# Kernel tuning notes

Hardware: AMD Instinct MI355X
Metric: run time of the kernel (lower is better)

The kernel has to match this reference:

```python
import jax, jax.numpy as jnp
import numpy as np

B, V, T = 8, 16, 64
DIN, H, RH, K, TMP = 6, 256, 64, 2, 256
E = V * (V - 1)
NREL, NPOS = 7, 3  # 2D relative / positional feature counts

_edges = np.ones((V, V)) - np.eye(V)
SEND = jnp.asarray(np.where(_edges)[0])
RECV = jnp.asarray(np.where(_edges)[1])


def _w(k, shape, fan):
    return jax.random.normal(k, shape, jnp.float32) / np.sqrt(fan)


def setup_inputs() -> dict:
    key = jax.random.key(0)
    ks = jax.random.split(key, 20)
    d = {}
    d['rel_feat'] = jax.random.normal(ks[0], (B, V, T, DIN), jnp.float32)
    d['edge_attr_raw'] = jax.random.normal(ks[1], (B, E, T, NREL + DIN), jnp.float32)
    d['edge_pos'] = jax.random.normal(ks[2], (B, E, T, NPOS), jnp.float32)
    d['ef_w1'] = _w(ks[3], (H, NREL + DIN + NPOS), NREL + DIN + NPOS); d['ef_b1'] = jnp.full((H,), 0.1)
    d['ef_w2'] = _w(ks[4], (H, H), H); d['ef_b2'] = jnp.full((H,), 0.1)
    d['res_w'] = _w(ks[5], (H, DIN), DIN); d['res_b'] = jnp.full((H,), 0.1)
    d['m3_w1'] = _w(ks[6], (H, H), H); d['m3_b1'] = jnp.full((H,), 0.1)
    d['m3_w2'] = _w(ks[7], (H, H), H); d['m3_b2'] = jnp.full((H,), 0.1)
    d['m4_w1'] = _w(ks[8], (H, 3 * H), 3 * H); d['m4_b1'] = jnp.full((H,), 0.1)
    d['m4_w2'] = _w(ks[9], (H, H), H); d['m4_b2'] = jnp.full((H,), 0.1)
    d['f_wih'] = _w(ks[10], (4 * RH, H), H); d['f_whh'] = _w(ks[11], (4 * RH, RH), RH)
    d['f_bih'] = jnp.zeros((4 * RH,)); d['f_bhh'] = jnp.zeros((4 * RH,))
    d['r_wih'] = _w(ks[12], (4 * RH, H), H); d['r_whh'] = _w(ks[13], (4 * RH, RH), RH)
    d['r_bih'] = jnp.zeros((4 * RH,)); d['r_bhh'] = jnp.zeros((4 * RH,))
    d['p_w'] = _w(ks[14], (K, RH), RH); d['p_b'] = jnp.full((K,), 0.1)
    d['e_w1'] = _w(ks[15], (TMP, 2 * RH), 2 * RH); d['e_b1'] = jnp.full((TMP,), 0.1)
    d['e_w2'] = _w(ks[16], (K, TMP), TMP); d['e_b2'] = jnp.full((K,), 0.1)
    return d


def _lstm(x, wih, whh, bih, bhh):
    # x: [N, T, H] -> hidden sequence [N, T, RH]; torch gate order i, f, g, o
    n = x.shape[0]
    rh = whh.shape[1]
    xw = jnp.einsum('nth,gh->ntg', x, wih) + bih  # input GEMM hoisted out of scan

    def step(carry, xt):
        h, c = carry
        z = xt + h @ whh.T + bhh
        i, f, g, o = jnp.split(z, 4, axis=-1)
        c = jax.nn.sigmoid(f) * c + jax.nn.sigmoid(i) * jnp.tanh(g)
        h = jax.nn.sigmoid(o) * jnp.tanh(c)
        return (h, c), h

    h0 = jnp.zeros((n, rh), x.dtype)
    _, hs = jax.lax.scan(step, (h0, h0), jnp.swapaxes(xw, 0, 1))
    return jnp.swapaxes(hs, 0, 1)


def reference(rel_feat, edge_attr_raw, edge_pos, ef_w1, ef_b1, ef_w2, ef_b2, res_w, res_b, m3_w1, m3_b1, m3_w2, m3_b2, m4_w1, m4_b1, m4_w2, m4_b2, f_wih, f_whh, f_bih, f_bhh, r_wih, r_whh, r_bih, r_bhh, p_w, p_b, e_w1, e_b1, e_w2, e_b2):
    elu = jax.nn.elu
    # edge filter MLP: [B,E,T,NREL+DIN+NPOS] -> [B,E,T,H]
    ein = jnp.concatenate([edge_attr_raw, edge_pos], -1)
    edge_attr = elu(elu(ein @ ef_w1.T + ef_b1) @ ef_w2.T + ef_b2)
    # edge2node: scatter-sum over recv indices, normalized by (V-1)
    agg = jax.ops.segment_sum(jnp.moveaxis(edge_attr, 1, 0), RECV, num_segments=V)
    x = jnp.moveaxis(agg, 0, 1) / (V - 1) + (rel_feat @ res_w.T + res_b)
    # mlp3 on node embeddings
    x = elu(elu(x @ m3_w1.T + m3_b1) @ m3_w2.T + m3_b2)
    # node2edge gather + skip-concat with previous edge features -> mlp4
    x = jnp.concatenate([x[:, SEND], x[:, RECV], edge_attr], -1)  # [B,E,T,3H]
    x = elu(elu(x @ m4_w1.T + m4_b1) @ m4_w2.T + m4_b2)  # [B,E,T,H]
    # bidirectional LSTM over time, per edge
    seq = x.reshape(B * E, T, H)
    fwd = _lstm(seq, f_wih, f_whh, f_bih, f_bhh)
    rev = jnp.flip(_lstm(jnp.flip(seq, 1), r_wih, r_whh, r_bih, r_bhh), 1)
    prior = (fwd @ p_w.T + p_b).reshape(B, E, T, K).transpose(0, 2, 1, 3)  # [B,T,E,K]
    comb = jnp.concatenate([fwd, rev], -1)
    enc = (elu(comb @ e_w1.T + e_b1) @ e_w2.T + e_b2).reshape(B, E, T, K).transpose(0, 2, 1, 3)
    return prior, enc
```

## Files before the change

kernel.cpp:

```cpp
#include <hip/hip_runtime.h>
#include <cstdint>
#include <cstddef>
#include <type_traits>

#define B_ 8
#define V_ 16
#define T_ 64
#define E_ 240
#define H_ 256
#define RH_ 64
#define K_ 2
#define DIN_ 6
#define BET_ (B_*E_*T_)
#define BVT_ (B_*V_*T_)
#define BE_ (B_*E_)

typedef unsigned short ushort_t;
typedef unsigned int u32;
typedef __attribute__((ext_vector_type(8))) short bf16x8;
typedef __attribute__((ext_vector_type(4))) float f32x4;

__device__ __forceinline__ float eluf(float x) { return x > 0.f ? x : __expf(x) - 1.f; }
__device__ __forceinline__ float fsig(float x) { return 1.f / (1.f + __expf(-x)); }
__device__ __forceinline__ float ftanh_(float x) {
    float y = fminf(fmaxf(x, -8.f), 8.f);
    float e = __expf(2.f * y);
    return (e - 1.f) / (e + 1.f);
}
__device__ __forceinline__ float b2f(ushort_t u) {
    union { float f; uint32_t i; } v; v.i = ((uint32_t)u) << 16; return v.f;
}
__device__ __forceinline__ ushort_t f2b(float f) {
    union { float f; uint32_t i; } v; v.f = f;
    uint32_t r = (v.i + 0x7FFFu + ((v.i >> 16) & 1u)) >> 16;
    return (ushort_t)r;
}

__device__ __forceinline__ void gll16(const void* g, void* l) {
    __builtin_amdgcn_global_load_lds(
        (const __attribute__((address_space(1))) u32*)g,
        (__attribute__((address_space(3))) u32*)l, 16, 0, 0);
}

template<int KD, int ACT>
__global__ __launch_bounds__(512, 2) void gemm8_k(
    const ushort_t* __restrict__ A, const ushort_t* __restrict__ Wt,
    const float* __restrict__ b1, const float* __restrict__ b2,
    ushort_t* __restrict__ C)
{
    __shared__ ushort_t lds[4][32][512];
    const int tid = threadIdx.x;
    const int lane = tid & 63;
    const int w = tid >> 6;
    const int wm = w >> 2, wn = w & 3;
    const int m0 = blockIdx.x * 256;
    const int r16 = lane & 15, kq = lane >> 4;
    constexpr int NH = KD / 32;

    const ushort_t* Ag0 = A + (size_t)(m0 + w * 16 + r16) * KD + kq * 8;
    const ushort_t* Ag1 = A + (size_t)(m0 + (w + 8) * 16 + r16) * KD + kq * 8;
    const ushort_t* Bg0 = Wt + (size_t)(w * 16 + r16) * KD + kq * 8;
    const ushort_t* Bg1 = Wt + (size_t)((w + 8) * 16 + r16) * KD + kq * 8;

    f32x4 acc[8][4];
    #pragma unroll
    for (int i = 0; i < 8; ++i)
        #pragma unroll
        for (int j = 0; j < 4; ++j)
            acc[i][j] = (f32x4){0.f, 0.f, 0.f, 0.f};

#define ST8(h) do { int sl_ = (h) & 3; int kk_ = (h) * 32;                  \
    gll16(Ag0 + kk_, &lds[sl_][w][0]);                                      \
    gll16(Ag1 + kk_, &lds[sl_][w + 8][0]);                                  \
    gll16(Bg0 + kk_, &lds[sl_][16 + w][0]);                                 \
    gll16(Bg1 + kk_, &lds[sl_][16 + w + 8][0]);                             \
} while (0)

    ST8(0); ST8(1); ST8(2);
    asm volatile("s_waitcnt vmcnt(8)" ::: "memory");
    __builtin_amdgcn_s_barrier();

    for (int h = 0; h < NH; ++h) {
        if (h + 3 < NH) ST8(h + 3);
        const int sl = h & 3;
        bf16x8 bfr[4];
        #pragma unroll
        for (int nf = 0; nf < 4; ++nf)
            bfr[nf] = *(const bf16x8*)&lds[sl][16 + wn * 4 + nf][lane * 8];
        #pragma unroll
        for (int mh = 0; mh < 2; ++mh) {
            bf16x8 af[4];
            #pragma unroll
            for (int mf = 0; mf < 4; ++mf)
                af[mf] = *(const bf16x8*)&lds[sl][wm * 8 + mh * 4 + mf][lane * 8];
            __builtin_amdgcn_s_setprio(1);
            #pragma unroll
            for (int mf = 0; mf < 4; ++mf)
                #pragma unroll
                for (int nf = 0; nf < 4; ++nf)
                    acc[mh * 4 + mf][nf] = __builtin_amdgcn_mfma_f32_16x16x32_bf16(
                        bfr[nf], af[mf], acc[mh * 4 + mf][nf], 0, 0, 0);
            __builtin_amdgcn_s_setprio(0);
        }
        asm volatile("s_waitcnt lgkmcnt(0)" ::: "memory");
        if (h < NH - 3)       { asm volatile("s_waitcnt vmcnt(8)" ::: "memory"); }
        else if (h == NH - 3) { asm volatile("s_waitcnt vmcnt(4)" ::: "memory"); }
        else if (h == NH - 2) { asm volatile("s_waitcnt vmcnt(0)" ::: "memory"); }
        if (h < NH - 1) __builtin_amdgcn_s_barrier();
    }
#undef ST8

    #pragma unroll
    for (int mi = 0; mi < 8; ++mi) {
        int mrow = m0 + wm * 128 + mi * 16 + r16;
        #pragma unroll
        for (int nf = 0; nf < 4; ++nf) {
            int nb = wn * 64 + nf * 16 + kq * 4;
            float4 bb = *(const float4*)&b1[nb];
            if (b2) {
                float4 b2v = *(const float4*)&b2[nb];
                bb.x += b2v.x; bb.y += b2v.y; bb.z += b2v.z; bb.w += b2v.w;
            }
            float v0 = acc[mi][nf][0] + bb.x;
            float v1 = acc[mi][nf][1] + bb.y;
            float v2 = acc[mi][nf][2] + bb.z;
            float v3 = acc[mi][nf][3] + bb.w;
            if (ACT) { v0 = eluf(v0); v1 = eluf(v1); v2 = eluf(v2); v3 = eluf(v3); }
            ushort4 o; o.x = f2b(v0); o.y = f2b(v1); o.z = f2b(v2); o.w = f2b(v3);
            *(ushort4*)&C[(size_t)mrow * 256 + nb] = o;
        }
    }
}

__global__ __launch_bounds__(512, 2) void gemm8_mlp4_k(
    const ushort_t* __restrict__ X2b, const ushort_t* __restrict__ EA,
    const ushort_t* __restrict__ Wt, const float* __restrict__ b1,
    ushort_t* __restrict__ C)
{
    __shared__ ushort_t lds[4][32][512];
    const int tid = threadIdx.x;
    const int lane = tid & 63;
    const int w = tid >> 6;
    const int wm = w >> 2, wn = w & 3;
    const int m0 = blockIdx.x * 256;
    const int r16 = lane & 15, kq = lane >> 4;
    constexpr int NH = 24;

    const ushort_t* AS[2]; const ushort_t* AR[2]; const ushort_t* AE[2];
    #pragma unroll
    for (int ff = 0; ff < 2; ++ff) {
        int f = w + ff * 8;
        int m = m0 + f * 16 + r16;
        int be = m >> 6, t = m & 63;
        int b = be / E_, e = be % E_;
        int s = e / (V_ - 1);
        int r0 = e % (V_ - 1);
        int rr = r0 + (r0 >= s ? 1 : 0);
        AS[ff] = X2b + ((size_t)((b * V_ + s) * T_ + t)) * H_ + kq * 8;
        AR[ff] = X2b + ((size_t)((b * V_ + rr) * T_ + t)) * H_ + kq * 8;
        AE[ff] = EA + (size_t)m * H_ + kq * 8;
    }
    const ushort_t* Bg0 = Wt + (size_t)(w * 16 + r16) * 768 + kq * 8;
    const ushort_t* Bg1 = Wt + (size_t)((w + 8) * 16 + r16) * 768 + kq * 8;

    f32x4 acc[8][4];
    #pragma unroll
    for (int i = 0; i < 8; ++i)
        #pragma unroll
        for (int j = 0; j < 4; ++j)
            acc[i][j] = (f32x4){0.f, 0.f, 0.f, 0.f};

#define STM(h) do { int sl_ = (h) & 3; int kk_ = (h) * 32;                  \
    int seg_ = kk_ >> 8, off_ = kk_ & 255;                                  \
    const ushort_t* a0_ = (seg_ == 0 ? AS[0] : seg_ == 1 ? AR[0] : AE[0]) + off_; \
    const ushort_t* a1_ = (seg_ == 0 ? AS[1] : seg_ == 1 ? AR[1] : AE[1]) + off_; \
    gll16(a0_, &lds[sl_][w][0]);                                            \
    gll16(a1_, &lds[sl_][w + 8][0]);                                        \
    gll16(Bg0 + kk_, &lds[sl_][16 + w][0]);                                 \
    gll16(Bg1 + kk_, &lds[sl_][16 + w + 8][0]);                             \
} while (0)

    STM(0); STM(1); STM(2);
    asm volatile("s_waitcnt vmcnt(8)" ::: "memory");
    __builtin_amdgcn_s_barrier();

    for (int h = 0; h < NH; ++h) {
        if (h + 3 < NH) STM(h + 3);
        const int sl = h & 3;
        bf16x8 bfr[4];
        #pragma unroll
        for (int nf = 0; nf < 4; ++nf)
            bfr[nf] = *(const bf16x8*)&lds[sl][16 + wn * 4 + nf][lane * 8];
        #pragma unroll
        for (int mh = 0; mh < 2; ++mh) {
            bf16x8 af[4];
            #pragma unroll
            for (int mf = 0; mf < 4; ++mf)
                af[mf] = *(const bf16x8*)&lds[sl][wm * 8 + mh * 4 + mf][lane * 8];
            __builtin_amdgcn_s_setprio(1);
            #pragma unroll
            for (int mf = 0; mf < 4; ++mf)
                #pragma unroll
                for (int nf = 0; nf < 4; ++nf)
                    acc[mh * 4 + mf][nf] = __builtin_amdgcn_mfma_f32_16x16x32_bf16(
                        bfr[nf], af[mf], acc[mh * 4 + mf][nf], 0, 0, 0);
            __builtin_amdgcn_s_setprio(0);
        }
        asm volatile("s_waitcnt lgkmcnt(0)" ::: "memory");
        if (h < NH - 3)       { asm volatile("s_waitcnt vmcnt(8)" ::: "memory"); }
        else if (h == NH - 3) { asm volatile("s_waitcnt vmcnt(4)" ::: "memory"); }
        else if (h == NH - 2) { asm volatile("s_waitcnt vmcnt(0)" ::: "memory"); }
        if (h < NH - 1) __builtin_amdgcn_s_barrier();
    }
#undef STM

    #pragma unroll
    for (int mi = 0; mi < 8; ++mi) {
        int mrow = m0 + wm * 128 + mi * 16 + r16;
        #pragma unroll
        for (int nf = 0; nf < 4; ++nf) {
            int nb = wn * 64 + nf * 16 + kq * 4;
            float4 bb = *(const float4*)&b1[nb];
            float v0 = eluf(acc[mi][nf][0] + bb.x);
            float v1 = eluf(acc[mi][nf][1] + bb.y);
            float v2 = eluf(acc[mi][nf][2] + bb.z);
            float v3 = eluf(acc[mi][nf][3] + bb.w);
            ushort4 o; o.x = f2b(v0); o.y = f2b(v1); o.z = f2b(v2); o.w = f2b(v3);
            *(ushort4*)&C[(size_t)mrow * 256 + nb] = o;
        }
    }
}

__global__ __launch_bounds__(256) void wconv_k(
    const float* __restrict__ ef_w2, const float* __restrict__ m4_w1,
    const float* __restrict__ m4_w2, const float* __restrict__ f_wih,
    const float* __restrict__ r_wih, const float* __restrict__ e_w1,
    ushort_t* __restrict__ Wb)
{
    int i = blockIdx.x * 256 + threadIdx.x;
    const float* src; int off;
    if (i < 65536)       { src = ef_w2; off = i; }
    else if (i < 262144) { src = m4_w1; off = i - 65536; }
    else if (i < 327680) { src = m4_w2; off = i - 262144; }
    else if (i < 393216) { src = f_wih; off = i - 327680; }
    else if (i < 458752) { src = r_wih; off = i - 393216; }
    else                 { src = e_w1;  off = i - 458752; }
    Wb[i] = f2b(src[off]);
}

template<typename TA, typename TO>
__global__ __launch_bounds__(256) void gemm_t(
    const TA* __restrict__ A, const float* __restrict__ W,
    const float* __restrict__ b1, const float* __restrict__ b2,
    TO* __restrict__ C, int M, int Kd, int N, int act)
{
    __shared__ float As[16][64];
    __shared__ float Ws[16][64];
    const int m0 = blockIdx.x * 64, n0 = blockIdx.y * 64;
    const int tid = threadIdx.x;
    const int tm = tid >> 4, tn = tid & 15;
    const int lm = tid >> 2, lq = tid & 3;
    float acc[4][4] = {};
    const TA* Arow = A + (size_t)(m0 + lm) * Kd + lq * 4;
    const float* Wrow = W + (size_t)(n0 + lm) * Kd + lq * 4;
    for (int k0 = 0; k0 < Kd; k0 += 16) {
        float4 av, wv;
        if constexpr (std::is_same<TA, ushort_t>::value) {
            ushort4 u = *(const ushort4*)(Arow + k0);
            av.x = b2f(u.x); av.y = b2f(u.y); av.z = b2f(u.z); av.w = b2f(u.w);
        } else {
            av = *(const float4*)(Arow + k0);
        }
        wv = *(const float4*)(Wrow + k0);
        __syncthreads();
        As[lq*4+0][lm] = av.x; As[lq*4+1][lm] = av.y; As[lq*4+2][lm] = av.z; As[lq*4+3][lm] = av.w;
        Ws[lq*4+0][lm] = wv.x; Ws[lq*4+1][lm] = wv.y; Ws[lq*4+2][lm] = wv.z; Ws[lq*4+3][lm] = wv.w;
        __syncthreads();
        #pragma unroll
        for (int k = 0; k < 16; ++k) {
            float4 a = *(const float4*)&As[k][tm * 4];
            float4 w = *(const float4*)&Ws[k][tn * 4];
            float a_[4] = {a.x, a.y, a.z, a.w};
            float w_[4] = {w.x, w.y, w.z, w.w};
            #pragma unroll
            for (int i = 0; i < 4; ++i)
                #pragma unroll
                for (int j = 0; j < 4; ++j)
                    acc[i][j] += a_[i] * w_[j];
        }
    }
    float bb[4];
    #pragma unroll
    for (int j = 0; j < 4; ++j) {
        int n = n0 + tn * 4 + j;
        bb[j] = b1[n] + (b2 ? b2[n] : 0.f);
    }
    #pragma unroll
    for (int i = 0; i < 4; ++i) {
        float v0 = acc[i][0] + bb[0], v1 = acc[i][1] + bb[1];
        float v2 = acc[i][2] + bb[2], v3 = acc[i][3] + bb[3];
        if (act) { v0 = eluf(v0); v1 = eluf(v1); v2 = eluf(v2); v3 = eluf(v3); }
        TO* dst = C + (size_t)(m0 + tm * 4 + i) * N + (n0 + tn * 4);
        if constexpr (std::is_same<TO, ushort_t>::value) {
            ushort4 o; o.x = f2b(v0); o.y = f2b(v1); o.z = f2b(v2); o.w = f2b(v3);
            *(ushort4*)dst = o;
        } else {
            float4 o; o.x = v0; o.y = v1; o.z = v2; o.w = v3;
            *(float4*)dst = o;
        }
    }
}

__global__ __launch_bounds__(256) void gemm_ein_k(
    const float* __restrict__ ear, const float* __restrict__ epos,
    const float* __restrict__ W, const float* __restrict__ b1,
    ushort_t* __restrict__ C)
{
    __shared__ float As[16][64];
    __shared__ float Ws[16][64];
    const int m0 = blockIdx.x * 64, n0 = blockIdx.y * 64;
    const int tid = threadIdx.x;
    const int tm = tid >> 4, tn = tid & 15;
    const int lm = tid >> 2, lq = tid & 3;
    const int m = m0 + lm;
    float a_[4];
    #pragma unroll
    for (int q = 0; q < 4; ++q) {
        int c = lq * 4 + q;
        a_[q] = (c < 13) ? ear[(size_t)m * 13 + c] : epos[(size_t)m * 3 + (c - 13)];
    }
    float4 wv = *(const float4*)(W + (size_t)(n0 + lm) * 16 + lq * 4);
    As[lq*4+0][lm] = a_[0]; As[lq*4+1][lm] = a_[1]; As[lq*4+2][lm] = a_[2]; As[lq*4+3][lm] = a_[3];
    Ws[lq*4+0][lm] = wv.x; Ws[lq*4+1][lm] = wv.y; Ws[lq*4+2][lm] = wv.z; Ws[lq*4+3][lm] = wv.w;
    __syncthreads();
    float acc[4][4] = {};
    #pragma unroll
    for (int k = 0; k < 16; ++k) {
        float4 a = *(const float4*)&As[k][tm * 4];
        float4 w = *(const float4*)&Ws[k][tn * 4];
        float aa[4] = {a.x, a.y, a.z, a.w};
        float ww[4] = {w.x, w.y, w.z, w.w};
        #pragma unroll
        for (int i = 0; i < 4; ++i)
            #pragma unroll
            for (int j = 0; j < 4; ++j)
                acc[i][j] += aa[i] * ww[j];
    }
    #pragma unroll
    for (int i = 0; i < 4; ++i) {
        ushort4 o;
        o.x = f2b(eluf(acc[i][0] + b1[n0 + tn*4 + 0]));
        o.y = f2b(eluf(acc[i][1] + b1[n0 + tn*4 + 1]));
        o.z = f2b(eluf(acc[i][2] + b1[n0 + tn*4 + 2]));
        o.w = f2b(eluf(acc[i][3] + b1[n0 + tn*4 + 3]));
        *(ushort4*)(C + (size_t)(m0 + tm * 4 + i) * H_ + (n0 + tn * 4)) = o;
    }
}

__global__ __launch_bounds__(256) void e2n_k(
    const ushort_t* __restrict__ EA, const float* __restrict__ rel,
    const float* __restrict__ res_w, const float* __restrict__ res_b,
    float* __restrict__ X)
{
    const int idx = blockIdx.x;
    const int t = idx & (T_ - 1);
    const int bv = idx >> 6;
    const int v = bv & (V_ - 1);
    const int b = bv >> 4;
    const int h = threadIdx.x;
    float sum = 0.f;
    #pragma unroll
    for (int i = 0; i < V_; ++i) {
        if (i == v) continue;
        int jj = (v < i) ? v : v - 1;
        int e = i * (V_ - 1) + jj;
        sum += b2f(EA[(((size_t)(b * E_ + e)) * T_ + t) * H_ + h]);
    }
    const float* rp = rel + ((size_t)bv * T_ + t) * DIN_;
    float res = res_b[h];
    #pragma unroll
    for (int d = 0; d < DIN_; ++d) res += rp[d] * res_w[h * DIN_ + d];
    X[((size_t)bv * T_ + t) * H_ + h] = sum * (1.f / 15.f) + res;
}

__global__ __launch_bounds__(256) void lstm_mfma4_k(
    const ushort_t* __restrict__ G, const float* __restrict__ whh,
    ushort_t* __restrict__ COMB, int dir)
{
    __shared__ ushort_t hlds[2][1024];
    const int tid = threadIdx.x;
    const int lane = tid & 63;
    const int w = tid >> 6;
    const int seq = lane & 15, kq = lane >> 4;
    const int be0 = blockIdx.x * 16;
    const int swz = (seq & 7) << 4;

    bf16x8 wf[4][2];
    #pragma unroll
    for (int a = 0; a < 4; ++a) {
        #pragma unroll
        for (int ks = 0; ks < 2; ++ks) {
            const float* p = whh + (size_t)((a * 4 + w) * 16 + seq) * 64 + ks * 32 + kq * 8;
            float4 x0 = *(const float4*)p;
            float4 x1 = *(const float4*)(p + 4);
            bf16x8 v;
            v[0] = (short)f2b(x0.x); v[1] = (short)f2b(x0.y);
            v[2] = (short)f2b(x0.z); v[3] = (short)f2b(x0.w);
            v[4] = (short)f2b(x1.x); v[5] = (short)f2b(x1.y);
            v[6] = (short)f2b(x1.z); v[7] = (short)f2b(x1.w);
            wf[a][ks] = v;
        }
    }

    const ushort_t* grow = G + ((size_t)(be0 + seq) * T_) * 256 + kq * 4;
    ushort_t* crow = COMB + ((size_t)(be0 + seq) * T_) * 128 + (dir ? 64 : 0) + 16 * w + 4 * kq;

    float c[4] = {};
    ushort4 gx[4];
    const int t0 = dir ? (T_ - 1) : 0;
    #pragma unroll
    for (int a = 0; a < 4; ++a)
        gx[a] = *(const ushort4*)(grow + (size_t)t0 * 256 + (a * 4 + w) * 16);

    for (int s = 0; s < T_; ++s) {
        const int t = dir ? (T_ - 1 - s) : s;
        f32x4 acc[4];
        #pragma unroll
        for (int a = 0; a < 4; ++a) {
            ushort4 g = gx[a];
            acc[a] = (f32x4){b2f(g.x), b2f(g.y), b2f(g.z), b2f(g.w)};
        }
        if (s < T_ - 1) {
            const int tn = dir ? (T_ - 2 - s) : (s + 1);
            #pragma unroll
            for (int a = 0; a < 4; ++a)
                gx[a] = *(const ushort4*)(grow + (size_t)tn * 256 + (a * 4 + w) * 16);
        }
        if (s) {
            bf16x8 af[2];
            #pragma unroll
            for (int ks = 0; ks < 2; ++ks) {
                int boff = (seq * 128 + ks * 64 + kq * 16) ^ swz;
                af[ks] = *(const bf16x8*)((const char*)hlds[(s - 1) & 1] + boff);
            }
            #pragma unroll
            for (int a = 0; a < 4; ++a) {
                acc[a] = __builtin_amdgcn_mfma_f32_16x16x32_bf16(wf[a][0], af[0], acc[a], 0, 0, 0);
                acc[a] = __builtin_amdgcn_mfma_f32_16x16x32_bf16(wf[a][1], af[1], acc[a], 0, 0, 0);
            }
        }
        float hh[4];
        #pragma unroll
        for (int r = 0; r < 4; ++r) {
            float zi = acc[0][r], zf = acc[1][r], zg = acc[2][r], zo = acc[3][r];
            float cc = fsig(zf) * c[r] + fsig(zi) * ftanh_(zg);
            c[r] = cc;
            hh[r] = fsig(zo) * ftanh_(cc);
        }
        ushort4 hv;
        hv.x = f2b(hh[0]); hv.y = f2b(hh[1]); hv.z = f2b(hh[2]); hv.w = f2b(hh[3]);
        int wb = (seq * 128 + 32 * w + 8 * kq) ^ swz;
        *(ushort4*)((char*)hlds[s & 1] + wb) = hv;
        *(ushort4*)(crow + (size_t)t * 128) = hv;
        asm volatile("s_waitcnt lgkmcnt(0)" ::: "memory");
        __builtin_amdgcn_sched_barrier(0);
        __builtin_amdgcn_s_barrier();
    }
}

__global__ __launch_bounds__(256) void prior_k(
    const ushort_t* __restrict__ COMB, const float* __restrict__ p_w,
    const float* __restrict__ p_b, float* __restrict__ out)
{
    const int row = blockIdx.x * 4 + (threadIdx.x >> 6);
    const int lane = threadIdx.x & 63;
    float hf = b2f(COMB[(size_t)row * 128 + lane]);
    float v0 = hf * p_w[lane];
    float v1 = hf * p_w[64 + lane];
    #pragma unroll
    for (int off = 32; off > 0; off >>= 1) {
        v0 += __shfl_down(v0, off, 64);
        v1 += __shfl_down(v1, off, 64);
    }
    if (lane == 0) {
        int t = row & (T_ - 1);
        int be = row >> 6;
        int e = be % E_, b = be / E_;
        size_t o = (((size_t)b * T_ + t) * E_ + e) * K_;
        out[o] = v0 + p_b[0];
        out[o + 1] = v1 + p_b[1];
    }
}

__global__ __launch_bounds__(512) void fused_enc_k(
    const ushort_t* __restrict__ COMB, const ushort_t* __restrict__ w_e1,
    const float* __restrict__ e_b1, const float* __restrict__ e_w2,
    const float* __restrict__ e_b2, float* __restrict__ out)
{
    __shared__ ushort_t sA[2][8][512];
    __shared__ ushort_t sW[2][16][512];
    __shared__ float part[128][4][2];
    const int tid = threadIdx.x;
    const int lane = tid & 63;
    const int w = tid >> 6;
    const int wr = w >> 2, wc = w & 3;
    const int m0 = blockIdx.x * 128;
    const int r16 = lane & 15, kq = lane >> 4;

    const ushort_t* Asrc = COMB + (size_t)(m0 + w * 16 + r16) * 128 + kq * 8;
    const size_t woffA = (size_t)((2 * w) * 16 + r16) * 128 + kq * 8;
    const size_t woffB = (size_t)((2 * w + 1) * 16 + r16) * 128 + kq * 8;

    float4 w2v[2][4];
    #pragma unroll
    for (int j = 0; j < 2; ++j)
        #pragma unroll
        for (int nf = 0; nf < 4; ++nf)
            w2v[j][nf] = *(const float4*)&e_w2[j * 256 + wc * 64 + nf * 16 + kq * 4];

    f32x4 acc[4][4];
    #pragma unroll
    for (int i = 0; i < 4; ++i)
        #pragma unroll
        for (int j = 0; j < 4; ++j)
            acc[i][j] = (f32x4){0.f, 0.f, 0.f, 0.f};

#define FE_STAGE(bufi, kt_) do {                                             \
    gll16(Asrc + (kt_) * 32, &sA[bufi][w][0]);                               \
    gll16(w_e1 + woffA + (kt_) * 32, &sW[bufi][2 * w][0]);                   \
    gll16(w_e1 + woffB + (kt_) * 32, &sW[bufi][2 * w + 1][0]);               \
} while (0)

    FE_STAGE(0, 0);
    asm volatile("s_waitcnt vmcnt(0)" ::: "memory");
    __builtin_amdgcn_s_barrier();

    for (int s = 0; s < 4; ++s) {
        const int buf = s & 1;
        if (s < 3) FE_STAGE(buf ^ 1, s + 1);
        bf16x8 af[4], bfr[4];
        #pragma unroll
        for (int mf = 0; mf < 4; ++mf)
            af[mf] = *(const bf16x8*)&sA[buf][wr * 4 + mf][lane * 8];
        #pragma unroll
        for (int nf = 0; nf < 4; ++nf)
            bfr[nf] = *(const bf16x8*)&sW[buf][wc * 4 + nf][lane * 8];
        #pragma unroll
        for (int mf = 0; mf < 4; ++mf)
            #pragma unroll
            for (int nf = 0; nf < 4; ++nf)
                acc[mf][nf] = __builtin_amdgcn_mfma_f32_16x16x32_bf16(bfr[nf], af[mf], acc[mf][nf], 0, 0, 0);
        asm volatile("s_waitcnt vmcnt(0)" ::: "memory");
        __builtin_amdgcn_s_barrier();
    }

    #pragma unroll
    for (int mf = 0; mf < 4; ++mf) {
        float s0 = 0.f, s1 = 0.f;
        #pragma unroll
        for (int nf = 0; nf < 4; ++nf) {
            int col = wc * 64 + nf * 16 + kq * 4;
            float4 bb = *(const float4*)&e_b1[col];
            float v0 = eluf(acc[mf][nf][0] + bb.x);
            float v1 = eluf(acc[mf][nf][1] + bb.y);
            float v2 = eluf(acc[mf][nf][2] + bb.z);
            float v3 = eluf(acc[mf][nf][3] + bb.w);
            s0 += v0 * w2v[0][nf].x + v1 * w2v[0][nf].y + v2 * w2v[0][nf].z + v3 * w2v[0][nf].w;
            s1 += v0 * w2v[1][nf].x + v1 * w2v[1][nf].y + v2 * w2v[1][nf].z + v3 * w2v[1][nf].w;
        }
        s0 += __shfl_xor(s0, 16, 64); s0 += __shfl_xor(s0, 32, 64);
        s1 += __shfl_xor(s1, 16, 64); s1 += __shfl_xor(s1, 32, 64);
        if (kq == 0) {
            part[wr * 64 + mf * 16 + r16][wc][0] = s0;
            part[wr * 64 + mf * 16 + r16][wc][1] = s1;
        }
    }
    __syncthreads();
    if (tid < 256) {
        int row = tid >> 1, k = tid & 1;
        float v = part[row][0][k] + part[row][1][k] + part[row][2][k] + part[row][3][k] + e_b2[k];
        int gr = m0 + row;
        int be = gr >> 6, t = gr & 63;
        int e = be % E_, b = be / E_;
        out[(size_t)(B_ * T_ * E_ * K_) + (((size_t)b * T_ + t) * E_ + e) * K_ + k] = v;
    }
#undef FE_STAGE
}

extern "C" void kernel_launch(void* const* d_in, const int* in_sizes, int n_in,
                              void* d_out, int out_size, void* d_ws, size_t ws_size,
                              hipStream_t stream)
{
    const float* rel    = (const float*)d_in[0];
    const float* ear    = (const float*)d_in[1];
    const float* epos   = (const float*)d_in[2];
    const float* ef_w1  = (const float*)d_in[3];
    const float* ef_b1  = (const float*)d_in[4];
    const float* ef_w2  = (const float*)d_in[5];
    const float* ef_b2  = (const float*)d_in[6];
    const float* res_w  = (const float*)d_in[7];
    const float* res_b  = (const float*)d_in[8];
    const float* m3_w1  = (const float*)d_in[9];
    const float* m3_b1  = (const float*)d_in[10];
    const float* m3_w2  = (const float*)d_in[11];
    const float* m3_b2  = (const float*)d_in[12];
    const float* m4_w1  = (const float*)d_in[13];
    const float* m4_b1  = (const float*)d_in[14];
    const float* m4_w2  = (const float*)d_in[15];
    const float* m4_b2  = (const float*)d_in[16];
    const float* f_wih  = (const float*)d_in[17];
    const float* f_whh  = (const float*)d_in[18];
    const float* f_bih  = (const float*)d_in[19];
    const float* f_bhh  = (const float*)d_in[20];
    const float* r_wih  = (const float*)d_in[21];
    const float* r_whh  = (const float*)d_in[22];
    const float* r_bih  = (const float*)d_in[23];
    const float* r_bhh  = (const float*)d_in[24];
    const float* p_w    = (const float*)d_in[25];
    const float* p_b    = (const float*)d_in[26];
    const float* e_w1   = (const float*)d_in[27];
    const float* e_b1   = (const float*)d_in[28];
    const float* e_w2   = (const float*)d_in[29];
    const float* e_b2   = (const float*)d_in[30];
    float* out = (float*)d_out;

    char* ws = (char*)d_ws;
    const size_t BIGB  = (size_t)BET_ * H_ * sizeof(ushort_t);
    const size_t COMBB = (size_t)BET_ * 128 * sizeof(ushort_t);
    const size_t X2BB  = (size_t)BVT_ * H_ * sizeof(ushort_t);
    ushort_t* R1   = (ushort_t*)(ws);
    ushort_t* R2   = (ushort_t*)(ws + BIGB);
    ushort_t* COMB = (ushort_t*)(ws + 2 * BIGB);
    ushort_t* X2b  = (ushort_t*)(ws + 2 * BIGB + COMBB);
    ushort_t* Wb   = (ushort_t*)(ws + 2 * BIGB + COMBB + X2BB);
    float* X  = (float*)(ws);
    float* XH = (float*)(ws + (size_t)BVT_ * H_ * sizeof(float));
    const ushort_t* wb_ef2  = Wb + 0;
    const ushort_t* wb_m41  = Wb + 65536;
    const ushort_t* wb_m42  = Wb + 262144;
    const ushort_t* wb_fwih = Wb + 327680;
    const ushort_t* wb_rwih = Wb + 393216;
    const ushort_t* wb_ew1  = Wb + 458752;

    dim3 blk(256);
    dim3 blk8(512);
    dim3 g8(BET_ / 256);
    dim3 gE64(BET_ / 64, 4);
    dim3 gN(BVT_ / 64, 4);

    wconv_k<<<1920, blk, 0, stream>>>(ef_w2, m4_w1, m4_w2, f_wih, r_wih, e_w1, Wb);
    gemm_ein_k<<<gE64, blk, 0, stream>>>(ear, epos, ef_w1, ef_b1, R1);
    gemm8_k<256, 1><<<g8, blk8, 0, stream>>>(R1, wb_ef2, ef_b2, nullptr, R2);
    e2n_k<<<BVT_, blk, 0, stream>>>(R2, rel, res_w, res_b, X);
    gemm_t<float, float><<<gN, blk, 0, stream>>>(X, m3_w1, m3_b1, nullptr, XH, BVT_, H_, H_, 1);
    gemm_t<float, ushort_t><<<gN, blk, 0, stream>>>(XH, m3_w2, m3_b2, nullptr, X2b, BVT_, H_, H_, 1);
    gemm8_mlp4_k<<<g8, blk8, 0, stream>>>(X2b, R2, wb_m41, m4_b1, R1);
    gemm8_k<256, 1><<<g8, blk8, 0, stream>>>(R1, wb_m42, m4_b2, nullptr, R2);
    gemm8_k<256, 0><<<g8, blk8, 0, stream>>>(R2, wb_fwih, f_bih, f_bhh, R1);
    lstm_mfma4_k<<<BE_ / 16, blk, 0, stream>>>(R1, f_whh, COMB, 0);
    gemm8_k<256, 0><<<g8, blk8, 0, stream>>>(R2, wb_rwih, r_bih, r_bhh, R1);
    lstm_mfma4_k<<<BE_ / 16, blk, 0, stream>>>(R1, r_whh, COMB, 1);
    prior_k<<<BET_ / 4, blk, 0, stream>>>(COMB, p_w, p_b, out);
    fused_enc_k<<<BET_ / 128, blk8, 0, stream>>>(COMB, wb_ew1, e_b1, e_w2, e_b2, out);
}
```

Before: 493.9 us.

## Fuse edge-filter MLP, mlp4 second layer with both LSTM input GEMMs, merge LSTM launches

Replaces the separate edge-filter first-layer GEMM and second-layer GEMM with one kernel that computes layer one with MFMA and keeps it in LDS. It also fuses the mlp4 second layer with the forward and reverse LSTM input-projection GEMMs, keeping the intermediate in LDS rather than writing it to global memory. The two LSTM direction launches are merged into a single grid with blockIdx.y selecting the direction. The aim is to cut global round-trips of 61k-row activation tensors and kernel launches, and to let both directions run concurrently. In exchange, tiles shrink to 128 rows with occupancy 1, and the fused kernel writes in place into its input buffer T1.

```diff
diff --git a/kernel.cpp b/kernel.cpp
--- a/kernel.cpp
+++ b/kernel.cpp
@@ -42,94 +42,273 @@
         (__attribute__((address_space(3))) u32*)l, 16, 0, 0);
 }
 
-template<int KD, int ACT>
-__global__ __launch_bounds__(512, 2) void gemm8_k(
-    const ushort_t* __restrict__ A, const ushort_t* __restrict__ Wt,
-    const float* __restrict__ b1, const float* __restrict__ b2,
-    ushort_t* __restrict__ C)
-{
-    __shared__ ushort_t lds[4][32][512];
+__global__ __launch_bounds__(512, 1) void gemm8_ef_k(
+    const float* __restrict__ ear, const float* __restrict__ epos,
+    const float* __restrict__ ef_w1, const float* __restrict__ ef_b1,
+    const ushort_t* __restrict__ w_ef2, const float* __restrict__ ef_b2,
+    ushort_t* __restrict__ EA)
+{
+    __shared__ ushort_t H1[8][8][512];
+    __shared__ ushort_t slotB[4][16][512];
     const int tid = threadIdx.x;
     const int lane = tid & 63;
     const int w = tid >> 6;
     const int wm = w >> 2, wn = w & 3;
-    const int m0 = blockIdx.x * 256;
+    const int m0 = blockIdx.x * 128;
     const int r16 = lane & 15, kq = lane >> 4;
-    constexpr int NH = KD / 32;
-
-    const ushort_t* Ag0 = A + (size_t)(m0 + w * 16 + r16) * KD + kq * 8;
-    const ushort_t* Ag1 = A + (size_t)(m0 + (w + 8) * 16 + r16) * KD + kq * 8;
-    const ushort_t* Bg0 = Wt + (size_t)(w * 16 + r16) * KD + kq * 8;
-    const ushort_t* Bg1 = Wt + (size_t)((w + 8) * 16 + r16) * KD + kq * 8;
-
-    f32x4 acc[8][4];
-    #pragma unroll
-    for (int i = 0; i < 8; ++i)
+
+    f32x4 acc[4][4];
+    #pragma unroll
+    for (int i = 0; i < 4; ++i)
         #pragma unroll
         for (int j = 0; j < 4; ++j)
             acc[i][j] = (f32x4){0.f, 0.f, 0.f, 0.f};
-
-#define ST8(h) do { int sl_ = (h) & 3; int kk_ = (h) * 32;                  \
-    gll16(Ag0 + kk_, &lds[sl_][w][0]);                                      \
-    gll16(Ag1 + kk_, &lds[sl_][w + 8][0]);                                  \
-    gll16(Bg0 + kk_, &lds[sl_][16 + w][0]);                                 \
-    gll16(Bg1 + kk_, &lds[sl_][16 + w + 8][0]);                             \
+    {
+        bf16x8 af[4], bfr[4];
+        #pragma unroll
+        for (int mf = 0; mf < 4; ++mf) {
+            int m = m0 + wm * 64 + mf * 16 + r16;
+            #pragma unroll
+            for (int e = 0; e < 8; ++e) {
+                float v = 0.f;
+                if (kq < 2) {
+                    int c = kq * 8 + e;
+                    v = (c < 13) ? ear[(size_t)m * 13 + c] : epos[(size_t)m * 3 + (c - 13)];
+                }
+                af[mf][e] = (short)f2b(v);
+            }
+        }
+        #pragma unroll
+        for (int nf = 0; nf < 4; ++nf) {
+            int n = wn * 64 + nf * 16 + r16;
+            #pragma unroll
+            for (int e = 0; e < 8; ++e) {
+                float v = 0.f;
+                if (kq < 2) v = ef_w1[(size_t)n * 16 + kq * 8 + e];
+                bfr[nf][e] = (short)f2b(v);
+            }
+        }
+        #pragma unroll
+        for (int mf = 0; mf < 4; ++mf)
+            #pragma unroll
+            for (int nf = 0; nf < 4; ++nf)
+                acc[mf][nf] = __builtin_amdgcn_mfma_f32_16x16x32_bf16(bfr[nf], af[mf], acc[mf][nf], 0, 0, 0);
+    }
+
+    const size_t bo0 = (size_t)(2 * w * 16 + r16) * 256 + kq * 8;
+    const size_t bo1 = (size_t)((2 * w + 1) * 16 + r16) * 256 + kq * 8;
+#define EF_ST(h) do { int sl_ = (h) & 3;                                    \
+    gll16(w_ef2 + bo0 + (h) * 32, &slotB[sl_][2 * w][0]);                   \
+    gll16(w_ef2 + bo1 + (h) * 32, &slotB[sl_][2 * w + 1][0]);               \
 } while (0)
 
-    ST8(0); ST8(1); ST8(2);
-    asm volatile("s_waitcnt vmcnt(8)" ::: "memory");
+    EF_ST(0); EF_ST(1); EF_ST(2);
+
+    #pragma unroll
+    for (int mf = 0; mf < 4; ++mf) {
+        #pragma unroll
+        for (int nf = 0; nf < 4; ++nf) {
+            int col = wn * 64 + nf * 16 + kq * 4;
+            float4 bb = *(const float4*)&ef_b1[col];
+            ushort4 o;
+            o.x = f2b(eluf(acc[mf][nf][0] + bb.x));
+            o.y = f2b(eluf(acc[mf][nf][1] + bb.y));
+            o.z = f2b(eluf(acc[mf][nf][2] + bb.z));
+            o.w = f2b(eluf(acc[mf][nf][3] + bb.w));
+            int ktw = wn * 2 + (nf >> 1);
+            int lanew = r16 + 16 * (((nf & 1) << 1) | (kq >> 1));
+            *(ushort4*)&H1[wm * 4 + mf][ktw][lanew * 8 + (kq & 1) * 4] = o;
+            acc[mf][nf] = (f32x4){0.f, 0.f, 0.f, 0.f};
+        }
+    }
+    asm volatile("s_waitcnt lgkmcnt(0)" ::: "memory");
+    asm volatile("s_waitcnt vmcnt(4)" ::: "memory");
     __builtin_amdgcn_s_barrier();
 
-    for (int h = 0; h < NH; ++h) {
-        if (h + 3 < NH) ST8(h + 3);
+    #pragma unroll
+    for (int h = 0; h < 8; ++h) {
+        if (h + 3 < 8) EF_ST(h + 3);
         const int sl = h & 3;
-        bf16x8 bfr[4];
+        bf16x8 af[4], bfr[4];
         #pragma unroll
         for (int nf = 0; nf < 4; ++nf)
-            bfr[nf] = *(const bf16x8*)&lds[sl][16 + wn * 4 + nf][lane * 8];
-        #pragma unroll
-        for (int mh = 0; mh < 2; ++mh) {
-            bf16x8 af[4];
+            bfr[nf] = *(const bf16x8*)&slotB[sl][wn * 4 + nf][lane * 8];
+        #pragma unroll
+        for (int mf = 0; mf < 4; ++mf)
+            af[mf] = *(const bf16x8*)&H1[wm * 4 + mf][h][lane * 8];
+        __builtin_amdgcn_s_setprio(1);
+        #pragma unroll
+        for (int mf = 0; mf < 4; ++mf)
+            #pragma unroll
+            for (int nf = 0; nf < 4; ++nf)
+                acc[mf][nf] = __builtin_amdgcn_mfma_f32_16x16x32_bf16(bfr[nf], af[mf], acc[mf][nf], 0, 0, 0);
+        __builtin_amdgcn_s_setprio(0);
+        asm volatile("s_waitcnt lgkmcnt(0)" ::: "memory");
+        if (h <= 4)      { asm volatile("s_waitcnt vmcnt(4)" ::: "memory"); }
+        else if (h == 5) { asm volatile("s_waitcnt vmcnt(2)" ::: "memory"); }
+        else if (h == 6) { asm volatile("s_waitcnt vmcnt(0)" ::: "memory"); }
+        if (h < 7) __builtin_amdgcn_s_barrier();
+    }
+#undef EF_ST
+
+    #pragma unroll
+    for (int mf = 0; mf < 4; ++mf) {
+        int row = m0 + wm * 64 + mf * 16 + r16;
+        #pragma unroll
+        for (int nf = 0; nf < 4; ++nf) {
+            int col = wn * 64 + nf * 16 + kq * 4;
+            float4 bb = *(const float4*)&ef_b2[col];
+            ushort4 o;
+            o.x = f2b(eluf(acc[mf][nf][0] + bb.x));
+            o.y = f2b(eluf(acc[mf][nf][1] + bb.y));
+            o.z = f2b(eluf(acc[mf][nf][2] + bb.z));
+            o.w = f2b(eluf(acc[mf][nf][3] + bb.w));
+            *(ushort4*)&EA[(size_t)row * 256 + col] = o;
+        }
+    }
+}
+
+__global__ __launch_bounds__(512, 1) void fused_gates8_k(
+    ushort_t* __restrict__ T1, ushort_t* __restrict__ GR,
+    const ushort_t* __restrict__ w_m42, const ushort_t* __restrict__ w_fih,
+    const ushort_t* __restrict__ w_rih, const float* __restrict__ m4_b2,
+    const float* __restrict__ f_bih, const float* __restrict__ f_bhh,
+    const float* __restrict__ r_bih, const float* __restrict__ r_bhh)
+{
+    __shared__ ushort_t M2[8][8][512];
+    __shared__ ushort_t slotA[3][8][512];
+    __shared__ ushort_t slotB[3][16][512];
+    const int tid = threadIdx.x;
+    const int lane = tid & 63;
+    const int w = tid >> 6;
+    const int wm = w >> 2, wn = w & 3;
+    const int m0 = blockIdx.x * 128;
+    const int r16 = lane & 15, kq = lane >> 4;
+
+    const ushort_t* Ag = T1 + (size_t)(m0 + w * 16 + r16) * 256 + kq * 8;
+    const size_t bo0 = (size_t)(2 * w * 16 + r16) * 256 + kq * 8;
+    const size_t bo1 = (size_t)((2 * w + 1) * 16 + r16) * 256 + kq * 8;
+
+    float4 bm4[4], bfv[4], brv[4];
+    #pragma unroll
+    for (int nf = 0; nf < 4; ++nf) {
+        int col = wn * 64 + nf * 16 + kq * 4;
+        bm4[nf] = *(const float4*)&m4_b2[col];
+        float4 a = *(const float4*)&f_bih[col];
+        float4 b = *(const float4*)&f_bhh[col];
+        bfv[nf] = (float4){a.x + b.x, a.y + b.y, a.z + b.z, a.w + b.w};
+        a = *(const float4*)&r_bih[col];
+        b = *(const float4*)&r_bhh[col];
+        brv[nf] = (float4){a.x + b.x, a.y + b.y, a.z + b.z, a.w + b.w};
+    }
+
+    f32x4 acc[4][4];
+    #pragma unroll
+    for (int i = 0; i < 4; ++i)
+        #pragma unroll
+        for (int j = 0; j < 4; ++j)
+            acc[i][j] = (f32x4){0.f, 0.f, 0.f, 0.f};
+
+#define FG_ST(h) do { int sl_ = (h) % 3;                                    \
+    if ((h) < 8) {                                                          \
+        gll16(Ag + (h) * 32, &slotA[sl_][w][0]);                            \
+        gll16(w_m42 + bo0 + (h) * 32, &slotB[sl_][2 * w][0]);               \
+        gll16(w_m42 + bo1 + (h) * 32, &slotB[sl_][2 * w + 1][0]);           \
+    } else {                                                                \
+        const ushort_t* Wp_ = ((h) < 16) ? w_fih : w_rih;                   \
+        int kk_ = ((h) & 7) * 32;                                           \
+        gll16(Wp_ + bo0 + kk_, &slotB[sl_][2 * w][0]);                      \
+        gll16(Wp_ + bo1 + kk_, &slotB[sl_][2 * w + 1][0]);                  \
+    } } while (0)
+
+    FG_ST(0); FG_ST(1);
+    asm volatile("s_waitcnt vmcnt(3)" ::: "memory");
+    __builtin_amdgcn_s_barrier();
+
+    #pragma unroll
+    for (int h = 0; h < 24; ++h) {
+        if (h + 2 < 24) FG_ST(h + 2);
+        const int sl = h % 3, kt = h & 7;
+        bf16x8 af[4], bfr[4];
+        #pragma unroll
+        for (int nf = 0; nf < 4; ++nf)
+            bfr[nf] = *(const bf16x8*)&slotB[sl][wn * 4 + nf][lane * 8];
+        if (h < 8) {
             #pragma unroll
             for (int mf = 0; mf < 4; ++mf)
-                af[mf] = *(const bf16x8*)&lds[sl][wm * 8 + mh * 4 + mf][lane * 8];
-            __builtin_amdgcn_s_setprio(1);
+                af[mf] = *(const bf16x8*)&slotA[sl][wm * 4 + mf][lane * 8];
+        } else {
             #pragma unroll
             for (int mf = 0; mf < 4; ++mf)
+                af[mf] = *(const bf16x8*)&M2[wm * 4 + mf][kt][lane * 8];
+        }
+        __builtin_amdgcn_s_setprio(1);
+        #pragma unroll
+        for (int mf = 0; mf < 4; ++mf)
+            #pragma unroll
+            for (int nf = 0; nf < 4; ++nf)
+                acc[mf][nf] = __builtin_amdgcn_mfma_f32_16x16x32_bf16(bfr[nf], af[mf], acc[mf][nf], 0, 0, 0);
+        __builtin_amdgcn_s_setprio(0);
+
+        if (h == 7) {
+            #pragma unroll
+            for (int mf = 0; mf < 4; ++mf) {
                 #pragma unroll
-                for (int nf = 0; nf < 4; ++nf)
-                    acc[mh * 4 + mf][nf] = __builtin_amdgcn_mfma_f32_16x16x32_bf16(
-                        bfr[nf], af[mf], acc[mh * 4 + mf][nf], 0, 0, 0);
-            __builtin_amdgcn_s_setprio(0);
-        }
+                for (int nf = 0; nf < 4; ++nf) {
+                    ushort4 o;
+                    o.x = f2b(eluf(acc[mf][nf][0] + bm4[nf].x));
+                    o.y = f2b(eluf(acc[mf][nf][1] + bm4[nf].y));
+                    o.z = f2b(eluf(acc[mf][nf][2] + bm4[nf].z));
+                    o.w = f2b(eluf(acc[mf][nf][3] + bm4[nf].w));
+                    int ktw = wn * 2 + (nf >> 1);
+                    int lanew = r16 + 16 * (((nf & 1) << 1) | (kq >> 1));
+                    *(ushort4*)&M2[wm * 4 + mf][ktw][lanew * 8 + (kq & 1) * 4] = o;
+                    acc[mf][nf] = (f32x4){0.f, 0.f, 0.f, 0.f};
+                }
+            }
+        }
+        if (h == 15) {
+            #pragma unroll
+            for (int mf = 0; mf < 4; ++mf) {
+                int row = m0 + wm * 64 + mf * 16 + r16;
+                #pragma unroll
+                for (int nf = 0; nf < 4; ++nf) {
+                    int col = wn * 64 + nf * 16 + kq * 4;
+                    ushort4 o;
+                    o.x = f2b(acc[mf][nf][0] + bfv[nf].x);
+                    o.y = f2b(acc[mf][nf][1] + bfv[nf].y);
+                    o.z = f2b(acc[mf][nf][2] + bfv[nf].z);
+                    o.w = f2b(acc[mf][nf][3] + bfv[nf].w);
+                    *(ushort4*)&T1[(size_t)row * 256 + col] = o;
+                    acc[mf][nf] = (f32x4){0.f, 0.f, 0.f, 0.f};
+                }
+            }
+        }
+        if (h == 23) {
+            #pragma unroll
+            for (int mf = 0; mf < 4; ++mf) {
+                int row = m0 + wm * 64 + mf * 16 + r16;
+                #pragma unroll
+                for (int nf = 0; nf < 4; ++nf) {
+                    int col = wn * 64 + nf * 16 + kq * 4;
+                    ushort4 o;
+                    o.x = f2b(acc[mf][nf][0] + brv[nf].x);
+                    o.y = f2b(acc[mf][nf][1] + brv[nf].y);
+                    o.z = f2b(acc[mf][nf][2] + brv[nf].z);
+                    o.w = f2b(acc[mf][nf][3] + brv[nf].w);
+                    *(ushort4*)&GR[(size_t)row * 256 + col] = o;
+                }
+            }
+        }
+
         asm volatile("s_waitcnt lgkmcnt(0)" ::: "memory");
-        if (h < NH - 3)       { asm volatile("s_waitcnt vmcnt(8)" ::: "memory"); }
-        else if (h == NH - 3) { asm volatile("s_waitcnt vmcnt(4)" ::: "memory"); }
-        else if (h == NH - 2) { asm volatile("s_waitcnt vmcnt(0)" ::: "memory"); }
-        if (h < NH - 1) __builtin_amdgcn_s_barrier();
-    }
-#undef ST8
-
-    #pragma unroll
-    for (int mi = 0; mi < 8; ++mi) {
-        int mrow = m0 + wm * 128 + mi * 16 + r16;
-        #pragma unroll
-        for (int nf = 0; nf < 4; ++nf) {
-            int nb = wn * 64 + nf * 16 + kq * 4;
-            float4 bb = *(const float4*)&b1[nb];
-            if (b2) {
-                float4 b2v = *(const float4*)&b2[nb];
-                bb.x += b2v.x; bb.y += b2v.y; bb.z += b2v.z; bb.w += b2v.w;
-            }
-            float v0 = acc[mi][nf][0] + bb.x;
-            float v1 = acc[mi][nf][1] + bb.y;
-            float v2 = acc[mi][nf][2] + bb.z;
-            float v3 = acc[mi][nf][3] + bb.w;
-            if (ACT) { v0 = eluf(v0); v1 = eluf(v1); v2 = eluf(v2); v3 = eluf(v3); }
-            ushort4 o; o.x = f2b(v0); o.y = f2b(v1); o.z = f2b(v2); o.w = f2b(v3);
-            *(ushort4*)&C[(size_t)mrow * 256 + nb] = o;
-        }
-    }
+        if (h == 15)      { asm volatile("s_waitcnt vmcnt(0)" ::: "memory"); }
+        else if (h <= 5)  { asm volatile("s_waitcnt vmcnt(3)" ::: "memory"); }
+        else if (h <= 21) { asm volatile("s_waitcnt vmcnt(2)" ::: "memory"); }
+        else if (h == 22) { asm volatile("s_waitcnt vmcnt(0)" ::: "memory"); }
+        if (h < 23) __builtin_amdgcn_s_barrier();
+    }
+#undef FG_ST
 }
 
 __global__ __launch_bounds__(512, 2) void gemm8_mlp4_k(
@@ -311,52 +490,6 @@
     }
 }
 
-__global__ __launch_bounds__(256) void gemm_ein_k(
-    const float* __restrict__ ear, const float* __restrict__ epos,
-    const float* __restrict__ W, const float* __restrict__ b1,
-    ushort_t* __restrict__ C)
-{
-    __shared__ float As[16][64];
-    __shared__ float Ws[16][64];
-    const int m0 = blockIdx.x * 64, n0 = blockIdx.y * 64;
-    const int tid = threadIdx.x;
-    const int tm = tid >> 4, tn = tid & 15;
-    const int lm = tid >> 2, lq = tid & 3;
-    const int m = m0 + lm;
-    float a_[4];
-    #pragma unroll
-    for (int q = 0; q < 4; ++q) {
-        int c = lq * 4 + q;
-        a_[q] = (c < 13) ? ear[(size_t)m * 13 + c] : epos[(size_t)m * 3 + (c - 13)];
-    }
-    float4 wv = *(const float4*)(W + (size_t)(n0 + lm) * 16 + lq * 4);
-    As[lq*4+0][lm] = a_[0]; As[lq*4+1][lm] = a_[1]; As[lq*4+2][lm] = a_[2]; As[lq*4+3][lm] = a_[3];
-    Ws[lq*4+0][lm] = wv.x; Ws[lq*4+1][lm] = wv.y; Ws[lq*4+2][lm] = wv.z; Ws[lq*4+3][lm] = wv.w;
-    __syncthreads();
-    float acc[4][4] = {};
-    #pragma unroll
-    for (int k = 0; k < 16; ++k) {
-        float4 a = *(const float4*)&As[k][tm * 4];
-        float4 w = *(const float4*)&Ws[k][tn * 4];
-        float aa[4] = {a.x, a.y, a.z, a.w};
-        float ww[4] = {w.x, w.y, w.z, w.w};
-        #pragma unroll
-        for (int i = 0; i < 4; ++i)
-            #pragma unroll
-            for (int j = 0; j < 4; ++j)
-                acc[i][j] += aa[i] * ww[j];
-    }
-    #pragma unroll
-    for (int i = 0; i < 4; ++i) {
-        ushort4 o;
-        o.x = f2b(eluf(acc[i][0] + b1[n0 + tn*4 + 0]));
-        o.y = f2b(eluf(acc[i][1] + b1[n0 + tn*4 + 1]));
-        o.z = f2b(eluf(acc[i][2] + b1[n0 + tn*4 + 2]));
-        o.w = f2b(eluf(acc[i][3] + b1[n0 + tn*4 + 3]));
-        *(ushort4*)(C + (size_t)(m0 + tm * 4 + i) * H_ + (n0 + tn * 4)) = o;
-    }
-}
-
 __global__ __launch_bounds__(256) void e2n_k(
     const ushort_t* __restrict__ EA, const float* __restrict__ rel,
     const float* __restrict__ res_w, const float* __restrict__ res_b,
@@ -384,10 +517,14 @@
 }
 
 __global__ __launch_bounds__(256) void lstm_mfma4_k(
-    const ushort_t* __restrict__ G, const float* __restrict__ whh,
-    ushort_t* __restrict__ COMB, int dir)
+    const ushort_t* __restrict__ Gf, const ushort_t* __restrict__ Gr,
+    const float* __restrict__ whh_f, const float* __restrict__ whh_r,
+    ushort_t* __restrict__ COMB)
 {
     __shared__ ushort_t hlds[2][1024];
+    const int dir = blockIdx.y;
+    const ushort_t* G = dir ? Gr : Gf;
+    const float* whh = dir ? whh_r : whh_f;
     const int tid = threadIdx.x;
     const int lane = tid & 63;
     const int w = tid >> 6;
@@ -644,22 +781,19 @@
 
     dim3 blk(256);
     dim3 blk8(512);
-    dim3 g8(BET_ / 256);
-    dim3 gE64(BET_ / 64, 4);
+    dim3 g128(BET_ / 128);
+    dim3 g256(BET_ / 256);
     dim3 gN(BVT_ / 64, 4);
 
     wconv_k<<<1920, blk, 0, stream>>>(ef_w2, m4_w1, m4_w2, f_wih, r_wih, e_w1, Wb);
-    gemm_ein_k<<<gE64, blk, 0, stream>>>(ear, epos, ef_w1, ef_b1, R1);
-    gemm8_k<256, 1><<<g8, blk8, 0, stream>>>(R1, wb_ef2, ef_b2, nullptr, R2);
+    gemm8_ef_k<<<g128, blk8, 0, stream>>>(ear, epos, ef_w1, ef_b1, wb_ef2, ef_b2, R2);
     e2n_k<<<BVT_, blk, 0, stream>>>(R2, rel, res_w, res_b, X);
     gemm_t<float, float><<<gN, blk, 0, stream>>>(X, m3_w1, m3_b1, nullptr, XH, BVT_, H_, H_, 1);
     gemm_t<float, ushort_t><<<gN, blk, 0, stream>>>(XH, m3_w2, m3_b2, nullptr, X2b, BVT_, H_, H_, 1);
-    gemm8_mlp4_k<<<g8, blk8, 0, stream>>>(X2b, R2, wb_m41, m4_b1, R1);
-    gemm8_k<256, 1><<<g8, blk8, 0, stream>>>(R1, wb_m42, m4_b2, nullptr, R2);
-    gemm8_k<256, 0><<<g8, blk8, 0, stream>>>(R2, wb_fwih, f_bih, f_bhh, R1);
-    lstm_mfma4_k<<<BE_ / 16, blk, 0, stream>>>(R1, f_whh, COMB, 0);
-    gemm8_k<256, 0><<<g8, blk8, 0, stream>>>(R2, wb_rwih, r_bih, r_bhh, R1);
-    lstm_mfma4_k<<<BE_ / 16, blk, 0, stream>>>(R1, r_whh, COMB, 1);
+    gemm8_mlp4_k<<<g256, blk8, 0, stream>>>(X2b, R2, wb_m41, m4_b1, R1);
+    fused_gates8_k<<<g128, blk8, 0, stream>>>(
+        R1, R2, wb_m42, wb_fwih, wb_rwih, m4_b2, f_bih, f_bhh, r_bih, r_bhh);
+    lstm_mfma4_k<<<dim3(BE_ / 16, 2), blk, 0, stream>>>(R1, R2, f_whh, r_whh, COMB);
     prior_k<<<BET_ / 4, blk, 0, stream>>>(COMB, p_w, p_b, out);
-    fused_enc_k<<<BET_ / 128, blk8, 0, stream>>>(COMB, wb_ew1, e_b1, e_w2, e_b2, out);
-}
+    fused_enc_k<<<g128, blk8, 0, stream>>>(COMB, wb_ew1, e_b1, e_w2, e_b2, out);
+}
```

Result: faster. 453.0 us (-8.3%).
